# Kernel optimization log

Hardware: AMD Instinct MI355X
Metric: run time of the kernel (lower is better)

## Reference

```python
import jax, jax.numpy as jnp
import numpy as np

B, L, IN, H, W = 4096, 10, 8, 512, 512


def setup_inputs() -> dict:
    key = jax.random.key(0)
    ks = jax.random.split(key, 24)
    s = 0.05  # small init so tanh/sigmoid stay in active range
    def rn(k, shape):
        return jax.random.normal(k, shape, dtype=jnp.float32) * s
    return {
        "items": jax.random.normal(ks[0], (B, L, IN), dtype=jnp.float32),
        "decoder_items_input": jax.random.uniform(ks[1], (B, H), dtype=jnp.float32),
        "emb_w": rn(ks[2], (H, IN)), "emb_b": rn(ks[3], (H,)),
        "enc_wih": rn(ks[4], (3 * H, H)), "enc_whh": rn(ks[5], (3 * H, H)),
        "enc_bih": rn(ks[6], (3 * H,)), "enc_bhh": rn(ks[7], (3 * H,)),
        "dec_wih": rn(ks[8], (3 * H, H)), "dec_whh": rn(ks[9], (3 * H, H)),
        "dec_bih": rn(ks[10], (3 * H,)), "dec_bhh": rn(ks[11], (3 * H,)),
        "w1": rn(ks[12], (W, H)), "w2": rn(ks[13], (W, H)),
        "w3": rn(ks[14], (W, H)), "w4": rn(ks[15], (W, H)),
        "w5": rn(ks[16], (W, H)), "w6": rn(ks[17], (W, H)),
        "w7": rn(ks[18], (W, 2 * H)),
        "v1": rn(ks[19], (W,)), "v2": rn(ks[20], (W,)),
        "v3_w": rn(ks[21], (W,)), "v3_b": rn(ks[22], (1,)),
        "wori": rn(ks[23], (6, 3 * H)), "bori": jnp.zeros((6,), jnp.float32),
    }


def _gru_scan(xg, whh, bhh, h0):
    # xg: [L,B,3H] precomputed input-gate projections; returns all hidden states [L,B,H]
    def step(h, xg_t):
        hg = h @ whh.T + bhh
        xr, xz, xn = jnp.split(xg_t, 3, axis=-1)
        hr, hz, hn = jnp.split(hg, 3, axis=-1)
        r = jax.nn.sigmoid(xr + hr)
        z = jax.nn.sigmoid(xz + hz)
        n = jnp.tanh(xn + r * hn)
        h_new = (1.0 - z) * n + z * h
        return h_new, h_new
    _, ys = jax.lax.scan(step, h0, xg)
    return ys


def _forward(items, decoder_items_input, emb_w, emb_b, enc_wih, enc_whh, enc_bih, enc_bhh,
             dec_wih, dec_whh, dec_bih, dec_bhh, w1, w2, w3, w4, w5, w6, w7,
             v1, v2, v3_w, v3_b, wori, bori):
    Bsz, Lln, _ = items.shape
    Hh = emb_w.shape[0]
    x = items @ emb_w.T + emb_b                                  # [B,L,H] embedding
    xg = (x @ enc_wih.T + enc_bih).transpose(1, 0, 2)            # [L,B,3H]
    enc_out = _gru_scan(xg, enc_whh, enc_bhh, jnp.zeros((Bsz, Hh), x.dtype))  # [L,B,H]
    h0 = enc_out[-1]                                             # last encoder state
    enc_blh = enc_out.transpose(1, 0, 2)                         # [B,L,H]
    enc_w3 = enc_out @ w3.T                                      # [L,B,W] (hoisted, step-invariant)
    enc_w6 = enc_out @ w6.T                                      # [L,B,W]
    xg_dec = decoder_items_input @ dec_wih.T + dec_bih           # [B,3H] constant decoder input
    xr, xz, xn = jnp.split(xg_dec, 3, axis=-1)

    def step(h, _):
        hg = h @ dec_whh.T + dec_bhh
        hr, hz, hn = jnp.split(hg, 3, axis=-1)
        r = jax.nn.sigmoid(xr + hr)
        z = jax.nn.sigmoid(xz + hz)
        n = jnp.tanh(xn + r * hn)
        h_new = (1.0 - z) * n + z * h                            # GRUCell update
        # intra attention cache is always length-1 in the source (the shape[1]==1 branch
        # always fires), so log_softmax is over a singleton axis -> exactly zero.
        doi = h_new[:, None, :]                                  # [B,1,H]
        oi = jnp.tanh(h_new @ w1.T + h_new @ w2.T) @ v1          # [B]
        attnd = jax.nn.log_softmax(oi[:, None, None], axis=-1)   # [B,1,1] zeros
        hi = (attnd * doi).sum(axis=1)                           # [B,H] (zeros, faithful)
        sm = jnp.tanh(enc_w3 + h_new @ w4.T + hi @ w5.T)         # [L,B,W]
        out_seq = (sm @ v2).T                                    # [B,L]
        sm_ori = jnp.tanh(enc_w6 + jnp.concatenate([h_new, hi], axis=-1) @ w7.T)  # [L,B,W]
        oo = sm_ori @ v3_w + v3_b[0]                             # [L,B]
        attnc = jax.nn.log_softmax(oo.T[:, :, None], axis=-1)    # [B,L,1] zeros (singleton axis)
        he = (attnc * enc_blh).sum(axis=1)                       # [B,H]
        total = jnp.concatenate([he, h_new, hi], axis=-1)        # [B,3H]
        out_ori = total @ wori.T + bori                          # [B,6]
        return h_new, (out_seq, out_ori)

    _, (seqs, oris) = jax.lax.scan(step, h0, None, length=Lln)
    probs_seq = seqs.transpose(1, 0, 2)                          # [B,L,L]
    probs_ori = oris.transpose(1, 0, 2)                          # [B,L,6]
    return probs_seq, probs_ori


def reference(items, decoder_items_input, emb_w, emb_b, enc_wih, enc_whh, enc_bih, enc_bhh,
              dec_wih, dec_whh, dec_bih, dec_bhh, w1, w2, w3, w4, w5, w6, w7,
              v1, v2, v3_w, v3_b, wori, bori):
    return _forward(items, decoder_items_input, emb_w, emb_b, enc_wih, enc_whh, enc_bih,
                    enc_bhh, dec_wih, dec_whh, dec_bih, dec_bhh, w1, w2, w3, w4, w5, w6,
                    w7, v1, v2, v3_w, v3_b, wori, bori)
```

## Files before the change

kernel.cpp:

```cpp
#include <hip/hip_runtime.h>
#include <hip/hip_bf16.h>


#define B_   4096
#define L_   10
#define IN_  8
#define H_   512
#define H3_  1536
#define W_   512
#define ORI_BASE (B_ * L_ * L_)

typedef __attribute__((ext_vector_type(8))) short s8v;
typedef __attribute__((ext_vector_type(4))) short s4v;
typedef __attribute__((ext_vector_type(4))) float f4v;

#define LOG2E  1.4426950408889634f
#define LOG2E2 2.8853900817779268f

__device__ __forceinline__ float sig_fast(float x) {
  float e = __builtin_amdgcn_exp2f(-x * LOG2E);
  return __builtin_amdgcn_rcpf(1.f + e);
}
__device__ __forceinline__ float tanh_fast(float x) {
  float e = __builtin_amdgcn_exp2f(x * LOG2E2);
  return 1.f - 2.f * __builtin_amdgcn_rcpf(e + 1.f);
}
__device__ __forceinline__ short f2bf(float f) {
  __hip_bfloat16 h = __float2bfloat16(f);
  return __builtin_bit_cast(short, h);
}
__device__ __forceinline__ float bf2f(short s) {
  __hip_bfloat16 h = __builtin_bit_cast(__hip_bfloat16, s);
  return __bfloat162float(h);
}
__device__ __forceinline__ void stc(float* p, float v) { *p = v; }
__device__ __forceinline__ void stc(short* p, float v) { *p = f2bf(v); }

__global__ __launch_bounds__(256) void prep_all(
    const float* __restrict__ s0, short* __restrict__ d0,
    const float* __restrict__ s1, short* __restrict__ d1,
    const float* __restrict__ s2, short* __restrict__ d2,
    const float* __restrict__ s3, short* __restrict__ d3,
    const float* __restrict__ s4, short* __restrict__ d4,
    const float* __restrict__ s5, short* __restrict__ d5)
{
  long i8 = (long)blockIdx.x * 256 + threadIdx.x;
  const float* s; short* d; long off;
  if      (i8 < 98304)  { s = s0; d = d0; off = i8; }
  else if (i8 < 196608) { s = s1; d = d1; off = i8 - 98304; }
  else if (i8 < 294912) { s = s2; d = d2; off = i8 - 196608; }
  else if (i8 < 327680) { s = s3; d = d3; off = i8 - 294912; }
  else if (i8 < 360448) { s = s4; d = d4; off = i8 - 327680; }
  else if (i8 < 622592) { s = s5; d = d5; off = i8 - 360448; }
  else return;
  const float* sp = s + off * 8;
  s8v v;
#pragma unroll
  for (int j = 0; j < 8; ++j) v[j] = f2bf(sp[j]);
  *(s8v*)(d + off * 8) = v;
}

__global__ __launch_bounds__(256) void build_wc(
    const float* __restrict__ enc_wih, const float* __restrict__ emb_w,
    const float* __restrict__ emb_b, const float* __restrict__ enc_bih,
    float* __restrict__ Wc, float* __restrict__ bc)
{
  __shared__ float se[H_ * IN_];
  __shared__ float sb[H_];
  const int tid = threadIdx.x;
  for (int i = tid; i < H_ * IN_; i += 256) se[i] = emb_w[i];
  for (int i = tid; i < H_; i += 256) sb[i] = emb_b[i];
  __syncthreads();
  int g = (blockIdx.x * 256 + tid) >> 6;
  int lane = tid & 63;
  const float* wr = enc_wih + (long)g * H_ + lane * 8;
  float w8[8];
#pragma unroll
  for (int j = 0; j < 8; ++j) w8[j] = wr[j];
  float acc[9] = {};
#pragma unroll
  for (int kk = 0; kk < 8; ++kk) {
    int k = lane * 8 + kk;
#pragma unroll
    for (int j = 0; j < 8; ++j) acc[j] += w8[kk] * se[k * IN_ + j];
    acc[8] += w8[kk] * sb[k];
  }
#pragma unroll
  for (int j = 0; j < 9; ++j)
#pragma unroll
    for (int off = 32; off; off >>= 1) acc[j] += __shfl_down(acc[j], off, 64);
  if (lane == 0) {
#pragma unroll
    for (int j = 0; j < 8; ++j) Wc[g * IN_ + j] = acc[j];
    bc[g] = acc[8] + enc_bih[g];
  }
}

template <typename CT>
__global__ __launch_bounds__(256) void gemm_bf16(
    const short* __restrict__ A, long lda,
    const short* __restrict__ Bw, long ldb,
    const float* __restrict__ bias,
    CT* __restrict__ C, long ldc, int K, float scale)
{
  __shared__ short As[2][128 * 64];
  __shared__ short Bs[2][128 * 64];
  const int tid = threadIdx.x;
  const long row0 = (long)blockIdx.y * 128;
  const long col0 = (long)blockIdx.x * 128;
  const int wave = tid >> 6, lane = tid & 63;
  const int wm = (wave & 1) * 64, wn = (wave >> 1) * 64;
  const int r16 = lane & 15, quad = lane >> 4;
  const int sw = r16 & 7;
  f4v acc[4][4] = {};

  auto stage = [&](int buf, int k0) {
#pragma unroll
    for (int r = 0; r < 4; ++r) {
      int idx = r * 256 + tid;
      int m = idx >> 3, c8 = idx & 7;
      int src = c8 ^ (m & 7);
      __builtin_amdgcn_global_load_lds(
          (const __attribute__((address_space(1))) void*)(A + (row0 + m) * lda + k0 + src * 8),
          (__attribute__((address_space(3))) void*)(&As[buf][idx * 8]), 16, 0, 0);
    }
#pragma unroll
    for (int r = 0; r < 4; ++r) {
      int idx = r * 256 + tid;
      int m = idx >> 3, c8 = idx & 7;
      int src = c8 ^ (m & 7);
      __builtin_amdgcn_global_load_lds(
          (const __attribute__((address_space(1))) void*)(Bw + (col0 + m) * ldb + k0 + src * 8),
          (__attribute__((address_space(3))) void*)(&Bs[buf][idx * 8]), 16, 0, 0);
    }
  };

  const int nk = K >> 6;
  stage(0, 0);
  for (int k = 0; k < nk; ++k) {
    if (k < nk - 1) {
      stage((k + 1) & 1, (k + 1) * 64);
      asm volatile("s_waitcnt vmcnt(8)" ::: "memory");
    } else {
      asm volatile("s_waitcnt vmcnt(0)" ::: "memory");
    }
    __builtin_amdgcn_s_barrier();
    const short* Asc = As[k & 1];
    const short* Bsc = Bs[k & 1];
    s8v af[4][2], bf[4][2];
#pragma unroll
    for (int i = 0; i < 4; ++i)
#pragma unroll
      for (int hh = 0; hh < 2; ++hh)
        af[i][hh] = *(const s8v*)&Asc[(wm + i * 16 + r16) * 64 + ((hh * 4 + quad) ^ sw) * 8];
#pragma unroll
    for (int j = 0; j < 4; ++j)
#pragma unroll
      for (int hh = 0; hh < 2; ++hh)
        bf[j][hh] = *(const s8v*)&Bsc[(wn + j * 16 + r16) * 64 + ((hh * 4 + quad) ^ sw) * 8];
    __builtin_amdgcn_s_setprio(1);
#pragma unroll
    for (int hh = 0; hh < 2; ++hh)
#pragma unroll
      for (int i = 0; i < 4; ++i)
#pragma unroll
        for (int j = 0; j < 4; ++j)
          acc[i][j] = __builtin_amdgcn_mfma_f32_16x16x32_bf16(af[i][hh], bf[j][hh], acc[i][j], 0, 0, 0);
    __builtin_amdgcn_s_setprio(0);
    __builtin_amdgcn_s_barrier();
  }

#pragma unroll
  for (int i = 0; i < 4; ++i) {
    long rbase = row0 + wm + i * 16 + quad * 4;
#pragma unroll
    for (int j = 0; j < 4; ++j) {
      long c = col0 + wn + j * 16 + r16;
      float bv = bias ? bias[c] : 0.f;
#pragma unroll
      for (int rg = 0; rg < 4; ++rg)
        stc(&C[(rbase + rg) * ldc + c], (acc[i][j][rg] + bv) * scale);
    }
  }
}

__global__ __launch_bounds__(256) void gemm_epi(
    const short* __restrict__ Ae, const short* __restrict__ Ad,
    const short* __restrict__ w3b, const short* __restrict__ w4b,
    short* __restrict__ Ce, short* __restrict__ Cd)
{
  const short* A  = blockIdx.z ? Ad : Ae;
  const short* Bw = blockIdx.z ? w4b : w3b;
  short* C        = blockIdx.z ? Cd : Ce;
  __shared__ short As[2][128 * 64];
  __shared__ short Bs[2][128 * 64];
  const int tid = threadIdx.x;
  const long row0 = (long)blockIdx.y * 128;
  const long col0 = (long)blockIdx.x * 128;
  const int wave = tid >> 6, lane = tid & 63;
  const int wm = (wave & 1) * 64, wn = (wave >> 1) * 64;
  const int r16 = lane & 15, quad = lane >> 4;
  const int sw = r16 & 7;
  f4v acc[4][4] = {};

  auto stage = [&](int buf, int k0) {
#pragma unroll
    for (int r = 0; r < 4; ++r) {
      int idx = r * 256 + tid;
      int m = idx >> 3, c8 = idx & 7;
      int src = c8 ^ (m & 7);
      __builtin_amdgcn_global_load_lds(
          (const __attribute__((address_space(1))) void*)(A + (row0 + m) * H_ + k0 + src * 8),
          (__attribute__((address_space(3))) void*)(&As[buf][idx * 8]), 16, 0, 0);
    }
#pragma unroll
    for (int r = 0; r < 4; ++r) {
      int idx = r * 256 + tid;
      int m = idx >> 3, c8 = idx & 7;
      int src = c8 ^ (m & 7);
      __builtin_amdgcn_global_load_lds(
          (const __attribute__((address_space(1))) void*)(Bw + (col0 + m) * H_ + k0 + src * 8),
          (__attribute__((address_space(3))) void*)(&Bs[buf][idx * 8]), 16, 0, 0);
    }
  };

  stage(0, 0);
  for (int k = 0; k < 8; ++k) {
    if (k < 7) {
      stage((k + 1) & 1, (k + 1) * 64);
      asm volatile("s_waitcnt vmcnt(8)" ::: "memory");
    } else {
      asm volatile("s_waitcnt vmcnt(0)" ::: "memory");
    }
    __builtin_amdgcn_s_barrier();
    const short* Asc = As[k & 1];
    const short* Bsc = Bs[k & 1];
    s8v af[4][2], bf[4][2];
#pragma unroll
    for (int i = 0; i < 4; ++i)
#pragma unroll
      for (int hh = 0; hh < 2; ++hh)
        af[i][hh] = *(const s8v*)&Asc[(wm + i * 16 + r16) * 64 + ((hh * 4 + quad) ^ sw) * 8];
#pragma unroll
    for (int j = 0; j < 4; ++j)
#pragma unroll
      for (int hh = 0; hh < 2; ++hh)
        bf[j][hh] = *(const s8v*)&Bsc[(wn + j * 16 + r16) * 64 + ((hh * 4 + quad) ^ sw) * 8];
    __builtin_amdgcn_s_setprio(1);
#pragma unroll
    for (int hh = 0; hh < 2; ++hh)
#pragma unroll
      for (int i = 0; i < 4; ++i)
#pragma unroll
        for (int j = 0; j < 4; ++j)
          acc[i][j] = __builtin_amdgcn_mfma_f32_16x16x32_bf16(af[i][hh], bf[j][hh], acc[i][j], 0, 0, 0);
    __builtin_amdgcn_s_setprio(0);
    __builtin_amdgcn_s_barrier();
  }

#pragma unroll
  for (int i = 0; i < 4; ++i) {
    long rbase = row0 + wm + i * 16 + quad * 4;
#pragma unroll
    for (int j = 0; j < 4; ++j) {
      long c = col0 + wn + j * 16 + r16;
#pragma unroll
      for (int rg = 0; rg < 4; ++rg)
        C[(rbase + rg) * W_ + c] = f2bf(acc[i][j][rg] * LOG2E2);
    }
  }
}

template <bool ENC>
__global__ __launch_bounds__(256) void gru_fused(
    const short* __restrict__ Aprev,
    const short* __restrict__ Whh,
    const float* __restrict__ bhh,
    const short* __restrict__ xg,
    const float* __restrict__ items_t,
    const float* __restrict__ Wc,
    const float* __restrict__ bc,
    short* __restrict__ hout)
{
  __shared__ short As[2][64 * 64];
  __shared__ short Bs[2][192 * 64];
  const int tid = threadIdx.x;
  const int flat = blockIdx.x;
  const int by = flat & 63, bx = flat >> 6;
  const long row0 = (long)by * 64;
  const int col0 = bx * 64;
  const int wave = tid >> 6, lane = tid & 63;
  const int r16 = lane & 15, quad = lane >> 4;
  const int sw = r16 & 7;

  f4v acc[3][4] = {};

  auto stage = [&](int buf, int k0) {
#pragma unroll
    for (int r = 0; r < 2; ++r) {
      int idx = r * 256 + tid;
      int m = idx >> 3, c8 = idx & 7;
      int src = c8 ^ (m & 7);
      __builtin_amdgcn_global_load_lds(
          (const __attribute__((address_space(1))) void*)(Aprev + (row0 + m) * H_ + k0 + src * 8),
          (__attribute__((address_space(3))) void*)(&As[buf][idx * 8]), 16, 0, 0);
    }
#pragma unroll
    for (int r = 0; r < 6; ++r) {
      int idx = r * 256 + tid;
      int m = idx >> 3, c8 = idx & 7;
      int src = c8 ^ (m & 7);
      int g = m >> 6, cc = m & 63;
      __builtin_amdgcn_global_load_lds(
          (const __attribute__((address_space(1))) void*)(Whh + ((long)g * H_ + col0 + cc) * H_ + k0 + src * 8),
          (__attribute__((address_space(3))) void*)(&Bs[buf][idx * 8]), 16, 0, 0);
    }
  };

  stage(0, 0);
  int cur = 0;
  for (int k = 0; k < 8; ++k) {
    if (k < 7) {
      stage(cur ^ 1, (k + 1) * 64);
      asm volatile("s_waitcnt vmcnt(8)" ::: "memory");
    } else {
      asm volatile("s_waitcnt vmcnt(0)" ::: "memory");
    }
    __builtin_amdgcn_s_barrier();
    s8v af[4][2], bf[3][2];
#pragma unroll
    for (int i = 0; i < 4; ++i)
#pragma unroll
      for (int hh = 0; hh < 2; ++hh)
        af[i][hh] = *(const s8v*)&As[cur][(i * 16 + r16) * 64 + ((hh * 4 + quad) ^ sw) * 8];
#pragma unroll
    for (int g = 0; g < 3; ++g)
#pragma unroll
      for (int hh = 0; hh < 2; ++hh)
        bf[g][hh] = *(const s8v*)&Bs[cur][(g * 64 + wave * 16 + r16) * 64 + ((hh * 4 + quad) ^ sw) * 8];
    __builtin_amdgcn_s_setprio(1);
#pragma unroll
    for (int hh = 0; hh < 2; ++hh)
#pragma unroll
      for (int g = 0; g < 3; ++g)
#pragma unroll
        for (int i = 0; i < 4; ++i)
          acc[g][i] = __builtin_amdgcn_mfma_f32_16x16x32_bf16(af[i][hh], bf[g][hh], acc[g][i], 0, 0, 0);
    __builtin_amdgcn_s_setprio(0);
    __builtin_amdgcn_s_barrier();
    cur ^= 1;
  }

  const int col = col0 + wave * 16 + r16;
  float wc[3][8], bcv[3];
  if (ENC) {
#pragma unroll
    for (int g = 0; g < 3; ++g) {
      const float* wr = Wc + ((long)g * H_ + col) * IN_;
#pragma unroll
      for (int j = 0; j < 8; ++j) wc[g][j] = wr[j];
      bcv[g] = bc[g * H_ + col];
    }
    float* itemS = (float*)As;
    int i2 = tid * 2;
    int m = i2 >> 3, j = i2 & 7;
    itemS[i2] = items_t[(row0 + m) * (L_ * IN_) + j];
    itemS[i2 + 1] = items_t[(row0 + m) * (L_ * IN_) + j + 1];
    __syncthreads();
  }
  float bhr = bhh[col], bhz = bhh[col + H_], bhn = bhh[col + 2 * H_];

#pragma unroll
  for (int i = 0; i < 4; ++i) {
#pragma unroll
    for (int rg = 0; rg < 4; ++rg) {
      int rl = i * 16 + quad * 4 + rg;
      long row = row0 + rl;
      float xr, xz, xn;
      if (ENC) {
        const float* it = (const float*)As + rl * 8;
        xr = bcv[0]; xz = bcv[1]; xn = bcv[2];
#pragma unroll
        for (int j = 0; j < 8; ++j) {
          float iv = it[j];
          xr += iv * wc[0][j];
          xz += iv * wc[1][j];
          xn += iv * wc[2][j];
        }
      } else {
        long gx = row * H3_ + col;
        xr = bf2f(xg[gx]); xz = bf2f(xg[gx + H_]); xn = bf2f(xg[gx + 2 * H_]);
      }
      float r = sig_fast(xr + acc[0][i][rg] + bhr);
      float z = sig_fast(xz + acc[1][i][rg] + bhz);
      float n = tanh_fast(xn + r * (acc[2][i][rg] + bhn));
      long hi = row * H_ + col;
      float hp = bf2f(Aprev[hi]);
      float hv = (1.f - z) * n + z * hp;
      hout[hi] = f2bf(hv);
    }
  }
}

__global__ __launch_bounds__(256) void out_seq_all(
    const short* __restrict__ ew3,
    const short* __restrict__ a4,
    const float* __restrict__ v2,
    float* __restrict__ out)
{
  __shared__ float se[L_ * W_];
  __shared__ float sa[L_ * W_];
  const int b = blockIdx.x;
  const int tid = threadIdx.x;
  for (int i = tid; i < L_ * 128; i += 256) {
    int row = i >> 7, q = i & 127;
    s4v ev = *(const s4v*)(ew3 + ((long)row * B_ + b) * W_ + q * 4);
    s4v av = *(const s4v*)(a4 + ((long)row * B_ + b) * W_ + q * 4);
    f4v e, a;
#pragma unroll
    for (int j = 0; j < 4; ++j) { e[j] = bf2f(ev[j]); a[j] = bf2f(av[j]); }
    *(f4v*)(se + row * W_ + q * 4) = e;
    *(f4v*)(sa + row * W_ + q * 4) = a;
  }
  const int wave = tid >> 6, lane = tid & 63;
  float sv0[4], sv1[4], svtot = 0.f;
#pragma unroll
  for (int q = 0; q < 4; ++q) {
    float v = v2[lane * 4 + q];
    sv0[q] = -2.f * v; svtot += v;
    v = v2[256 + lane * 4 + q];
    sv1[q] = -2.f * v; svtot += v;
  }
#pragma unroll
  for (int off = 32; off; off >>= 1) svtot += __shfl_down(svtot, off, 64);
  svtot = __shfl(svtot, 0, 64);
  __syncthreads();

  int tprev = -1;
  f4v a0, a1;
#pragma unroll
  for (int pp = 0; pp < 25; ++pp) {
    int p = wave * 25 + pp;
    int t = p / L_, l = p - t * L_;
    if (t != tprev) {
      a0 = *(const f4v*)(sa + t * W_ + lane * 4);
      a1 = *(const f4v*)(sa + t * W_ + 256 + lane * 4);
      tprev = t;
    }
    f4v e0 = *(const f4v*)(se + l * W_ + lane * 4);
    f4v e1 = *(const f4v*)(se + l * W_ + 256 + lane * 4);
    float acc = 0.f;
#pragma unroll
    for (int q = 0; q < 4; ++q) {
      float x0 = __builtin_amdgcn_exp2f(e0[q] + a0[q]);
      acc += sv0[q] * __builtin_amdgcn_rcpf(x0 + 1.f);
      float x1 = __builtin_amdgcn_exp2f(e1[q] + a1[q]);
      acc += sv1[q] * __builtin_amdgcn_rcpf(x1 + 1.f);
    }
#pragma unroll
    for (int off = 32; off; off >>= 1) acc += __shfl_down(acc, off, 64);
    if (lane == 0) out[((long)b * L_ + t) * L_ + l] = svtot + acc;
  }
}

__global__ __launch_bounds__(256) void out_ori_all(
    const short* __restrict__ dh,
    const float* __restrict__ wori, const float* __restrict__ bori,
    float* __restrict__ out)
{
  int wid = (blockIdx.x * 256 + threadIdx.x) >> 6;
  int lane = threadIdx.x & 63;
  int b = wid / L_, t = wid - b * L_;
  s8v hv = *(const s8v*)(dh + ((long)t * B_ + b) * H_ + lane * 8);
  float hf[8];
#pragma unroll
  for (int j = 0; j < 8; ++j) hf[j] = bf2f(hv[j]);
  float res[6];
#pragma unroll
  for (int o = 0; o < 6; ++o) {
    const float* wr = wori + (long)o * H3_ + H_ + lane * 8;
    float acc = 0.f;
#pragma unroll
    for (int j = 0; j < 8; ++j) acc += hf[j] * wr[j];
#pragma unroll
    for (int off = 32; off; off >>= 1) acc += __shfl_down(acc, off, 64);
    res[o] = acc;
  }
  if (lane == 0) {
    float* po = out + ORI_BASE + ((long)b * L_ + t) * 6;
#pragma unroll
    for (int o = 0; o < 6; ++o) po[o] = res[o] + bori[o];
  }
}

extern "C" void kernel_launch(void* const* d_in, const int* in_sizes, int n_in,
                              void* d_out, int out_size, void* d_ws, size_t ws_size,
                              hipStream_t stream)
{
  const float* items   = (const float*)d_in[0];
  const float* dec_in  = (const float*)d_in[1];
  const float* emb_w   = (const float*)d_in[2];
  const float* emb_b   = (const float*)d_in[3];
  const float* enc_wih = (const float*)d_in[4];
  const float* enc_whh = (const float*)d_in[5];
  const float* enc_bih = (const float*)d_in[6];
  const float* enc_bhh = (const float*)d_in[7];
  const float* dec_wih = (const float*)d_in[8];
  const float* dec_whh = (const float*)d_in[9];
  const float* dec_bih = (const float*)d_in[10];
  const float* dec_bhh = (const float*)d_in[11];
  const float* w3      = (const float*)d_in[14];
  const float* w4      = (const float*)d_in[15];
  const float* v2      = (const float*)d_in[20];
  const float* wori    = (const float*)d_in[23];
  const float* bori    = (const float*)d_in[24];
  float* out = (float*)d_out;

  char* ws = (char*)d_ws;
  size_t off = 0;
  auto alloc = [&](size_t bytes) { size_t o = off; off += (bytes + 255) & ~255UL; return o; };
  float* Wc       = (float*)(ws + alloc(H3_ * IN_ * 4));
  float* bc       = (float*)(ws + alloc(H3_ * 4));
  short* xgb      = (short*)(ws + alloc((size_t)B_ * H3_ * 2));
  short* enc_hist = (short*)(ws + alloc((size_t)11 * B_ * H_ * 2));
  short* dec_hist = (short*)(ws + alloc((size_t)L_ * B_ * H_ * 2));
  short* ew3      = (short*)(ws + alloc((size_t)L_ * B_ * W_ * 2));
  short* a4       = (short*)(ws + alloc((size_t)L_ * B_ * W_ * 2));
  short* whh_e    = (short*)(ws + alloc((size_t)H3_ * H_ * 2));
  short* whh_d    = (short*)(ws + alloc((size_t)H3_ * H_ * 2));
  short* wih_d    = (short*)(ws + alloc((size_t)H3_ * H_ * 2));
  short* w3b      = (short*)(ws + alloc((size_t)W_ * H_ * 2));
  short* w4b      = (short*)(ws + alloc((size_t)W_ * H_ * 2));
  short* decb     = (short*)(ws + alloc((size_t)B_ * H_ * 2));

  prep_all<<<(622592 + 255) / 256, 256, 0, stream>>>(
      enc_whh, whh_e, dec_whh, whh_d, dec_wih, wih_d,
      w3, w3b, w4, w4b, dec_in, decb);
  build_wc<<<384, 256, 0, stream>>>(enc_wih, emb_w, emb_b, enc_bih, Wc, bc);

  hipMemsetAsync(enc_hist, 0, (size_t)B_ * H_ * 2, stream);

  gemm_bf16<short><<<dim3(12, 32), 256, 0, stream>>>(
      decb, H_, wih_d, H_, dec_bih, xgb, H3_, H_, 1.f);

  for (int t = 0; t < L_; ++t) {
    gru_fused<true><<<512, 256, 0, stream>>>(
        enc_hist + (size_t)t * B_ * H_, whh_e, enc_bhh, nullptr,
        items + (size_t)t * IN_, Wc, bc,
        enc_hist + (size_t)(t + 1) * B_ * H_);
  }

  for (int t = 0; t < L_; ++t) {
    const short* prev = (t == 0) ? enc_hist + (size_t)10 * B_ * H_
                                 : dec_hist + (size_t)(t - 1) * B_ * H_;
    gru_fused<false><<<512, 256, 0, stream>>>(
        prev, whh_d, dec_bhh, xgb, nullptr, nullptr, nullptr,
        dec_hist + (size_t)t * B_ * H_);
  }

  gemm_epi<<<dim3(4, 320, 2), 256, 0, stream>>>(
      enc_hist + (size_t)B_ * H_, dec_hist, w3b, w4b, ew3, a4);
  out_seq_all<<<B_, 256, 0, stream>>>(ew3, a4, v2, out);
  out_ori_all<<<(B_ * L_) / 4, 256, 0, stream>>>(dec_hist, wori, bori, out);
}
```

Before: 534.1 us.

## Reduce out_seq attention dot products with bf16 MFMA over swizzled bf16 LDS

Rewrites the out_seq_all kernel so the encoder and decoder projections stay in LDS as bf16 with an XOR swizzle, instead of being widened to fp32. Each sigmoid tile is packed to bf16 and dotted with v2 through 16x16x32 bf16 MFMA instructions, replacing the per-pair wave shuffle reductions. Per-wave partial sums are then combined through a small shared buffer. This halves LDS footprint and traffic and removes the many shuffle reductions, at the cost of rounding the sigmoid outputs and v2 to bf16, which can loosen accuracy.

```diff
diff --git a/kernel.cpp b/kernel.cpp
--- a/kernel.cpp
+++ b/kernel.cpp
@@ -408,58 +408,88 @@
     const float* __restrict__ v2,
     float* __restrict__ out)
 {
-  __shared__ float se[L_ * W_];
-  __shared__ float sa[L_ * W_];
+  __shared__ short s_e[L_ * W_];
+  __shared__ short s_a[L_ * W_];
+  __shared__ short v2b[W_];
+  __shared__ float part[7 * 4 * 4 * 4];
+  __shared__ float svtot_s;
   const int b = blockIdx.x;
   const int tid = threadIdx.x;
-  for (int i = tid; i < L_ * 128; i += 256) {
-    int row = i >> 7, q = i & 127;
-    s4v ev = *(const s4v*)(ew3 + ((long)row * B_ + b) * W_ + q * 4);
-    s4v av = *(const s4v*)(a4 + ((long)row * B_ + b) * W_ + q * 4);
-    f4v e, a;
-#pragma unroll
-    for (int j = 0; j < 4; ++j) { e[j] = bf2f(ev[j]); a[j] = bf2f(av[j]); }
-    *(f4v*)(se + row * W_ + q * 4) = e;
-    *(f4v*)(sa + row * W_ + q * 4) = a;
-  }
-  const int wave = tid >> 6, lane = tid & 63;
-  float sv0[4], sv1[4], svtot = 0.f;
-#pragma unroll
-  for (int q = 0; q < 4; ++q) {
-    float v = v2[lane * 4 + q];
-    sv0[q] = -2.f * v; svtot += v;
-    v = v2[256 + lane * 4 + q];
-    sv1[q] = -2.f * v; svtot += v;
-  }
-#pragma unroll
-  for (int off = 32; off; off >>= 1) svtot += __shfl_down(svtot, off, 64);
-  svtot = __shfl(svtot, 0, 64);
+  const int w = tid >> 6, lane = tid & 63;
+  const int r16 = lane & 15, quad = lane >> 4;
+
+  for (int i = tid; i < L_ * 64; i += 256) {
+    int row = i >> 6, c = i & 63;
+    int swc = (c ^ (row & 7)) * 8;
+    *(s8v*)(s_e + row * W_ + swc) = *(const s8v*)(ew3 + ((long)row * B_ + b) * W_ + c * 8);
+    *(s8v*)(s_a + row * W_ + swc) = *(const s8v*)(a4  + ((long)row * B_ + b) * W_ + c * 8);
+  }
+  {
+    int i = tid * 2;
+    v2b[i] = f2bf(v2[i]);
+    v2b[i + 1] = f2bf(v2[i + 1]);
+  }
+  if (w == 0) {
+    float s = 0.f;
+    const float* vp = v2 + lane * 8;
+#pragma unroll
+    for (int j = 0; j < 8; ++j) s += vp[j];
+#pragma unroll
+    for (int off = 32; off; off >>= 1) s += __shfl_down(s, off, 64);
+    if (lane == 0) svtot_s = s;
+  }
   __syncthreads();
 
-  int tprev = -1;
-  f4v a0, a1;
-#pragma unroll
-  for (int pp = 0; pp < 25; ++pp) {
-    int p = wave * 25 + pp;
-    int t = p / L_, l = p - t * L_;
-    if (t != tprev) {
-      a0 = *(const f4v*)(sa + t * W_ + lane * 4);
-      a1 = *(const f4v*)(sa + t * W_ + 256 + lane * 4);
-      tprev = t;
-    }
-    f4v e0 = *(const f4v*)(se + l * W_ + lane * 4);
-    f4v e1 = *(const f4v*)(se + l * W_ + 256 + lane * 4);
-    float acc = 0.f;
-#pragma unroll
-    for (int q = 0; q < 4; ++q) {
-      float x0 = __builtin_amdgcn_exp2f(e0[q] + a0[q]);
-      acc += sv0[q] * __builtin_amdgcn_rcpf(x0 + 1.f);
-      float x1 = __builtin_amdgcn_exp2f(e1[q] + a1[q]);
-      acc += sv1[q] * __builtin_amdgcn_rcpf(x1 + 1.f);
-    }
-#pragma unroll
-    for (int off = 32; off; off >>= 1) acc += __shfl_down(acc, off, 64);
-    if (lane == 0) out[((long)b * L_ + t) * L_ + l] = svtot + acc;
+  s8v vfrag[4];
+#pragma unroll
+  for (int j = 0; j < 4; ++j)
+    vfrag[j] = *(const s8v*)(v2b + (w * 4 + j) * 32 + quad * 8);
+
+  f4v acc[7] = {};
+#pragma unroll
+  for (int g = 0; g < 7; ++g) {
+    int p = g * 16 + r16;
+    int t = (p * 205) >> 11;
+    int l = p - t * 10;
+    if (t > 9) t = 9;
+    const short* ep = s_e + l * W_;
+    const short* ap = s_a + t * W_;
+    const int le = l & 7, ta = t & 7;
+#pragma unroll
+    for (int j = 0; j < 4; ++j) {
+      int cb = (w * 4 + j) * 4 + quad;
+      s8v ev = *(const s8v*)(ep + (cb ^ le) * 8);
+      s8v av = *(const s8v*)(ap + (cb ^ ta) * 8);
+      s8v sf;
+#pragma unroll
+      for (int e = 0; e < 8; ++e) {
+        float x = bf2f(ev[e]) + bf2f(av[e]);
+        float s = __builtin_amdgcn_rcpf(__builtin_amdgcn_exp2f(x) + 1.f);
+        sf[e] = f2bf(s);
+      }
+      acc[g] = __builtin_amdgcn_mfma_f32_16x16x32_bf16(sf, vfrag[j], acc[g], 0, 0, 0);
+    }
+  }
+
+  if (r16 == 0) {
+#pragma unroll
+    for (int g = 0; g < 7; ++g)
+      *(f4v*)(part + ((g * 4 + quad) * 4 + w) * 4) = acc[g];
+  }
+  __syncthreads();
+  if (tid < 112) {
+    int g = tid >> 4, row = tid & 15;
+    int q = row >> 2, rg = row & 3;
+    float s = 0.f;
+#pragma unroll
+    for (int ww = 0; ww < 4; ++ww)
+      s += part[((g * 4 + q) * 4 + ww) * 4 + rg];
+    int p = g * 16 + row;
+    if (p < 100) {
+      int t = (p * 205) >> 11;
+      int l = p - t * 10;
+      out[((long)b * L_ + t) * L_ + l] = svtot_s - 2.f * s;
+    }
   }
 }
 
```

Result: no change. 530.8 us (-0.6%).
